# Kernel optimization log

Measured on AMD Instinct MI355X. Metric: run time of the kernel, lower is better.

## Reference

```python
import jax, jax.numpy as jnp
import numpy as np

SIZE = 512          # framebuffer resolution (init kwarg `size`)
NUM_TRIS = 512      # number of triangles
EPS = 1e-9          # degenerate-triangle area threshold (matches `w < 1e-09`)


def setup_inputs() -> dict:
    key = jax.random.key(0)
    tris = jax.random.normal(key, (NUM_TRIS, 3, 3), dtype=jnp.float32)
    return {"tris": tris}


def _area2d(a, b, c):
    # signed parallelogram area: (b.x-a.x)*(c.y-a.y) - (b.y-a.y)*(c.x-a.x)
    return (b[..., 0] - a[..., 0]) * (c[..., 1] - a[..., 1]) - \
           (b[..., 1] - a[..., 1]) * (c[..., 0] - a[..., 0])


def reference(tris):
    size = SIZE
    dtype = tris.dtype
    half = jnp.asarray(size, dtype) * 0.5

    # lookup_table: pts[i, j] = (x_i, y_j), linspace(-1, 1), 'ij' indexing
    lin = jnp.linspace(-1.0, 1.0, size, dtype=dtype)
    xx, yy = jnp.meshgrid(lin, lin, indexing="ij")
    pts = jnp.stack([xx, yy], axis=-1)              # [S, S, 2]
    ii = jnp.arange(size)[:, None]                  # row index
    jj = jnp.arange(size)[None, :]                  # col index

    # zmin = min over all vertices of the z coordinate
    zmin = tris.reshape(-1, 3).min(axis=0)[2]
    zbuf0 = jnp.full((size, size), zmin, dtype=dtype)
    res0 = jnp.zeros((size, size, 4), dtype=dtype)

    def step(carry, tri):
        zbuf, res = carry
        t2 = tri[:, :2]                              # [3, 2] screen-space verts

        # AABB -> integer pixel box: clamp to [-1,1], map to [0,size], floor (long cast)
        aabb = jnp.concatenate([t2.min(axis=0), t2.max(axis=0)])  # xmin,ymin,xmax,ymax
        idx = jnp.floor((jnp.clip(aabb, -1.0, 1.0) + 1.0) * half).astype(jnp.int32)
        xmin, ymin, xmax, ymax = idx[0], idx[1], idx[2], idx[3]
        box = (ii >= xmin) & (ii < xmax) & (jj >= ymin) & (jj < ymax)

        w = _area2d(t2[0], t2[1], t2[2])
        valid = w >= EPS                              # original: skip if w < 1e-9
        ws = jnp.where(valid, w, jnp.asarray(1.0, dtype))

        # edge functions over the whole grid (the AABB slice only restricts pixels;
        # `box` reproduces that restriction exactly)
        pAB = _area2d(t2[1], pts, t2[0])
        pCB = _area2d(t2[2], pts, t2[1])
        pCA = _area2d(t2[0], pts, t2[2])
        inside = (jnp.maximum(pAB, 0.0) * jnp.maximum(pCB, 0.0) * jnp.maximum(pCA, 0.0)) > 0

        # barycentric interpolation of the 3d vertices
        w1 = pCB / ws
        w2 = pCA / ws
        w3 = 1.0 - w1 - w2
        p3 = w1[..., None] * tri[0] + w2[..., None] * tri[1] + w3[..., None] * tri[2]  # [S,S,3]

        zmsk = p3[..., 2] >= zbuf
        rmsk = inside & zmsk & box & valid

        zbuf = jnp.where(rmsk, p3[..., 2], zbuf)
        rgba = jnp.concatenate([p3, jnp.ones_like(p3[..., :1])], axis=-1)  # [S,S,4]
        res = jnp.where(rmsk[..., None], rgba, res)
        return (zbuf, res), None

    (zbuf, res), _ = jax.lax.scan(step, (zbuf0, res0), tris)
    return res
```

## Files before the change

### kernel.cpp

```cpp
#include <hip/hip_runtime.h>

#define TSIZE 512
#define NT 512
#define EPSV 1e-9f


__device__ __forceinline__ float rcp_fast(float x) {
  float r;
  asm("v_rcp_f32 %0, %1" : "=v"(r) : "v"(x));
  return r;
}

__global__ __launch_bounds__(512) void render_fused(const float* __restrict__ tris,
                                                    float4* __restrict__ out) {
  __shared__ float4 lrec[NT * 4];
  __shared__ unsigned lbY[NT];
  __shared__ float2 smrg[NT];
  __shared__ float sred[8];

  const int tid = threadIdx.x;
  const int s = blockIdx.x;
  const int i = s >> 3;
  const unsigned jw0 = (unsigned)((s & 7) << 6);
  const float delta = 2.0f / 511.0f;

  {
    const float4* g4 = (const float4*)tris;
    float4* rw4 = lrec;
    rw4[tid] = g4[tid];
    rw4[tid + 512] = g4[tid + 512];
    int i3 = tid + 1024;
    if (i3 < 1152) rw4[i3] = g4[i3];
  }
  __syncthreads();

  const float* rawf = (const float*)lrec;
  const float* tp = rawf + tid * 9;
  float v0x = tp[0], v0y = tp[1], v0z = tp[2];
  float v1x = tp[3], v1y = tp[4], v1z = tp[5];
  float v2x = tp[6], v2y = tp[7], v2z = tp[8];
  __syncthreads();

  float w = __fsub_rn(__fmul_rn(__fsub_rn(v1x, v0x), __fsub_rn(v2y, v0y)),
                      __fmul_rn(__fsub_rn(v1y, v0y), __fsub_rn(v2x, v0x)));
  bool valid = (w >= EPSV);
  float ws = valid ? w : 1.0f;
  float r2  = __fsub_rn(v0y, v1y), r3  = __fsub_rn(v0x, v1x);
  float r6  = __fsub_rn(v1y, v2y), r7  = __fsub_rn(v1x, v2x);
  float r10 = __fsub_rn(v2y, v0y), r11 = __fsub_rn(v2x, v0x);

  int xmn = 0, xmx = 0, ymn = 0, ymx = 0;
  if (valid) {
    float bxn = fminf(v0x, fminf(v1x, v2x));
    float byn = fminf(v0y, fminf(v1y, v2y));
    float bxx = fmaxf(v0x, fmaxf(v1x, v2x));
    float byx = fmaxf(v0y, fmaxf(v1y, v2y));
    xmn = (int)floorf(__fmul_rn(__fadd_rn(fminf(fmaxf(bxn, -1.0f), 1.0f), 1.0f), 256.0f));
    ymn = (int)floorf(__fmul_rn(__fadd_rn(fminf(fmaxf(byn, -1.0f), 1.0f), 1.0f), 256.0f));
    xmx = (int)floorf(__fmul_rn(__fadd_rn(fminf(fmaxf(bxx, -1.0f), 1.0f), 1.0f), 256.0f));
    ymx = (int)floorf(__fmul_rn(__fadd_rn(fminf(fmaxf(byx, -1.0f), 1.0f), 1.0f), 256.0f));
  }

  bool pass = ((unsigned)i >= (unsigned)xmn) & ((unsigned)i < (unsigned)xmx) &
              ((unsigned)ymn < jw0 + 64u) & ((unsigned)ymx > jw0);
  if (pass) {
    const float px_s = -1.0f + (float)i * delta;
    const float pyL = -1.0f + (float)jw0 * delta;
    const float pyR = -1.0f + (float)(jw0 + 63u) * delta;
    float ylo = -1e30f, yhi = 1e30f;
    {
      float S = -r3, c = (v1y * r3 - v1x * r2) + r2 * px_s;
      if (S > 1e-20f)       { float cd = -c * rcp_fast(S); ylo = fmaxf(ylo, cd - (0.005f + 4e-6f * fabsf(cd))); }
      else if (S < -1e-20f) { float cd = -c * rcp_fast(S); yhi = fminf(yhi, cd + (0.005f + 4e-6f * fabsf(cd))); }
    }
    {
      float S = -r7, c = (v2y * r7 - v2x * r6) + r6 * px_s;
      if (S > 1e-20f)       { float cd = -c * rcp_fast(S); ylo = fmaxf(ylo, cd - (0.005f + 4e-6f * fabsf(cd))); }
      else if (S < -1e-20f) { float cd = -c * rcp_fast(S); yhi = fminf(yhi, cd + (0.005f + 4e-6f * fabsf(cd))); }
    }
    {
      float S = -r11, c = (v0y * r11 - v0x * r10) + r10 * px_s;
      if (S > 1e-20f)       { float cd = -c * rcp_fast(S); ylo = fmaxf(ylo, cd - (0.005f + 4e-6f * fabsf(cd))); }
      else if (S < -1e-20f) { float cd = -c * rcp_fast(S); yhi = fminf(yhi, cd + (0.005f + 4e-6f * fabsf(cd))); }
    }
    pass = (ylo <= pyR) & (yhi >= pyL);
  }
  const unsigned long long word = __ballot(pass ? 1 : 0);

  lrec[tid * 4 + 0] = make_float4(v1x, v1y, r2, r3);
  lrec[tid * 4 + 1] = make_float4(v2x, v2y, r6, r7);
  lrec[tid * 4 + 2] = make_float4(v0x, v0y, r10, r11);
  lrec[tid * 4 + 3] = make_float4(__fdiv_rn(1.0f, ws), v2z,
                                  __fsub_rn(v0z, v2z), __fsub_rn(v1z, v2z));
  lbY[tid] = (unsigned)ymn | ((unsigned)ymx << 16);

  float zp = fminf(v0z, fminf(v1z, v2z));
  for (int off = 32; off > 0; off >>= 1) zp = fminf(zp, __shfl_down(zp, off, 64));
  if ((tid & 63) == 0) sred[tid >> 6] = zp;
  __syncthreads();
  float zm0 = sred[0];
#pragma unroll
  for (int k = 1; k < 8; ++k) zm0 = fminf(zm0, sred[k]);

  const int lane = tid & 63;
  const int base = tid & ~63;
  const unsigned ju = jw0 + (unsigned)lane;
  const float px = __fadd_rn(-1.0f, __fmul_rn((float)i, delta));
  const float py = __fadd_rn(-1.0f, __fmul_rn((float)ju, delta));

  float zb = zm0;
  int tw = -1;
  unsigned long long m = word;
  while (m) {
    const int t = base + __builtin_ctzll(m);
    m &= m - 1;
    float4 c0 = lrec[t * 4 + 0];
    float4 c1 = lrec[t * 4 + 1];
    float4 c2 = lrec[t * 4 + 2];
    float4 c3 = lrec[t * 4 + 3];
    unsigned yb = lbY[t];
    float pAB = __fsub_rn(__fmul_rn(__fsub_rn(px, c0.x), c0.z),
                          __fmul_rn(__fsub_rn(py, c0.y), c0.w));
    float pCB = __fsub_rn(__fmul_rn(__fsub_rn(px, c1.x), c1.z),
                          __fmul_rn(__fsub_rn(py, c1.y), c1.w));
    float pCA = __fsub_rn(__fmul_rn(__fsub_rn(px, c2.x), c2.z),
                          __fmul_rn(__fsub_rn(py, c2.y), c2.w));
    bool ins = (pAB > 0.0f) & (pCB > 0.0f) & (pCA > 0.0f) &
               (ju >= (yb & 0xFFFFu)) & (ju < (yb >> 16));
    float w1 = __fmul_rn(pCB, c3.x);
    float w2 = __fmul_rn(pCA, c3.x);
    float pz = __fmaf_rn(w1, c3.z, __fmaf_rn(w2, c3.w, c3.y));
    bool mk = ins & (pz >= zb);
    zb = mk ? pz : zb;
    tw = mk ? t : tw;
  }
  smrg[tid] = make_float2(zb, __int_as_float(tw));
  __syncthreads();

  if (tid < 64) {
    float2 best = smrg[tid];
    float zf = best.x;
    int twf = __float_as_int(best.y);
#pragma unroll
    for (int w8 = 1; w8 < 8; ++w8) {
      float2 c = smrg[w8 * 64 + tid];
      int tc = __float_as_int(c.y);
      bool win = (c.x > zf) | ((c.x == zf) & (tc > twf));
      zf = win ? c.x : zf;
      twf = win ? tc : twf;
    }
    float4 res = make_float4(0.0f, 0.0f, 0.0f, 0.0f);
    if (twf >= 0) {
      float4 f1 = lrec[twf * 4 + 1];
      float4 f2 = lrec[twf * 4 + 2];
      float4 f3 = lrec[twf * 4 + 3];
      float pCB = __fsub_rn(__fmul_rn(__fsub_rn(px, f1.x), f1.z),
                            __fmul_rn(__fsub_rn(py, f1.y), f1.w));
      float pCA = __fsub_rn(__fmul_rn(__fsub_rn(px, f2.x), f2.z),
                            __fmul_rn(__fsub_rn(py, f2.y), f2.w));
      float w1 = __fmul_rn(pCB, f3.x);
      float w2 = __fmul_rn(pCA, f3.x);
      float rx = __fmaf_rn(w1, -f2.w, __fmaf_rn(w2, f1.w, f1.x));
      float ry = __fmaf_rn(w1, -f2.z, __fmaf_rn(w2, f1.z, f1.y));
      res = make_float4(rx, ry, zf, 1.0f);
    }
    out[((unsigned)i << 9) | (jw0 + (unsigned)tid)] = res;
  }
}

extern "C" void kernel_launch(void* const* d_in, const int* in_sizes, int n_in,
                              void* d_out, int out_size, void* d_ws, size_t ws_size,
                              hipStream_t stream) {
  const float* tris = (const float*)d_in[0];
  float4* out = (float4*)d_out;
  hipLaunchKernelGGL(render_fused, dim3(4096), dim3(512), 0, stream, tris, out);
}
```

Baseline: 78.49 us.

## Process 256 columns per block, splitting triangles across two waves per segment

Each block now covers half a row (256 pixels, four 64-pixel segments) instead of 64 pixels. Per-triangle setup and the triangle load into shared memory are amortized over four times as many pixels, and the grid shrinks from 4096 to 1024 blocks. Two waves share each segment and each handles half the triangles, so the final depth merge compares two candidates instead of eight. In exchange, per-wave work becomes more uneven and there are fewer blocks to hide latency.

Result: faster. 70.78 us (-9.8%).

```diff
diff --git a/kernel.cpp b/kernel.cpp
--- a/kernel.cpp
+++ b/kernel.cpp
@@ -16,12 +16,14 @@
   __shared__ float4 lrec[NT * 4];
   __shared__ unsigned lbY[NT];
   __shared__ float2 smrg[NT];
+  __shared__ unsigned long long swords[32];
   __shared__ float sred[8];
 
   const int tid = threadIdx.x;
-  const int s = blockIdx.x;
-  const int i = s >> 3;
-  const unsigned jw0 = (unsigned)((s & 7) << 6);
+  const int bb = blockIdx.x;
+  const int i = bb >> 1;
+  const int jhalf = bb & 1;
+  const unsigned jbase = (unsigned)(jhalf << 8);
   const float delta = 2.0f / 511.0f;
 
   {
@@ -29,8 +31,7 @@
     float4* rw4 = lrec;
     rw4[tid] = g4[tid];
     rw4[tid + 512] = g4[tid + 512];
-    int i3 = tid + 1024;
-    if (i3 < 1152) rw4[i3] = g4[i3];
+    if (tid < 128) rw4[tid + 1024] = g4[tid + 1024];
   }
   __syncthreads();
 
@@ -61,13 +62,10 @@
     ymx = (int)floorf(__fmul_rn(__fadd_rn(fminf(fmaxf(byx, -1.0f), 1.0f), 1.0f), 256.0f));
   }
 
-  bool pass = ((unsigned)i >= (unsigned)xmn) & ((unsigned)i < (unsigned)xmx) &
-              ((unsigned)ymn < jw0 + 64u) & ((unsigned)ymx > jw0);
-  if (pass) {
+  const bool xpass = ((unsigned)i >= (unsigned)xmn) & ((unsigned)i < (unsigned)xmx);
+  float ylo = -1e30f, yhi = 1e30f;
+  if (xpass) {
     const float px_s = -1.0f + (float)i * delta;
-    const float pyL = -1.0f + (float)jw0 * delta;
-    const float pyR = -1.0f + (float)(jw0 + 63u) * delta;
-    float ylo = -1e30f, yhi = 1e30f;
     {
       float S = -r3, c = (v1y * r3 - v1x * r2) + r2 * px_s;
       if (S > 1e-20f)       { float cd = -c * rcp_fast(S); ylo = fmaxf(ylo, cd - (0.005f + 4e-6f * fabsf(cd))); }
@@ -83,9 +81,18 @@
       if (S > 1e-20f)       { float cd = -c * rcp_fast(S); ylo = fmaxf(ylo, cd - (0.005f + 4e-6f * fabsf(cd))); }
       else if (S < -1e-20f) { float cd = -c * rcp_fast(S); yhi = fminf(yhi, cd + (0.005f + 4e-6f * fabsf(cd))); }
     }
-    pass = (ylo <= pyR) & (yhi >= pyL);
   }
-  const unsigned long long word = __ballot(pass ? 1 : 0);
+
+#pragma unroll
+  for (int k = 0; k < 4; ++k) {
+    const unsigned jw0 = jbase + ((unsigned)k << 6);
+    const float pyL = -1.0f + (float)jw0 * delta;
+    const float pyR = -1.0f + (float)(jw0 + 63u) * delta;
+    bool pk = xpass & ((unsigned)ymn < jw0 + 64u) & ((unsigned)ymx > jw0) &
+              (ylo <= pyR) & (yhi >= pyL);
+    unsigned long long wd = __ballot(pk ? 1 : 0);
+    if ((tid & 63) == 0) swords[k * 8 + (tid >> 6)] = wd;
+  }
 
   lrec[tid * 4 + 0] = make_float4(v1x, v1y, r2, r3);
   lrec[tid * 4 + 1] = make_float4(v2x, v2y, r6, r7);
@@ -100,71 +107,77 @@
   __syncthreads();
   float zm0 = sred[0];
 #pragma unroll
-  for (int k = 1; k < 8; ++k) zm0 = fminf(zm0, sred[k]);
+  for (int kk = 1; kk < 8; ++kk) zm0 = fminf(zm0, sred[kk]);
 
+  const int wv = tid >> 6;
   const int lane = tid & 63;
-  const int base = tid & ~63;
-  const unsigned ju = jw0 + (unsigned)lane;
+  const int k = wv >> 1;
+  const int h = wv & 1;
+  const unsigned ju = jbase + ((unsigned)k << 6) + (unsigned)lane;
   const float px = __fadd_rn(-1.0f, __fmul_rn((float)i, delta));
   const float py = __fadd_rn(-1.0f, __fmul_rn((float)ju, delta));
 
   float zb = zm0;
   int tw = -1;
-  unsigned long long m = word;
-  while (m) {
-    const int t = base + __builtin_ctzll(m);
-    m &= m - 1;
-    float4 c0 = lrec[t * 4 + 0];
-    float4 c1 = lrec[t * 4 + 1];
-    float4 c2 = lrec[t * 4 + 2];
-    float4 c3 = lrec[t * 4 + 3];
-    unsigned yb = lbY[t];
-    float pAB = __fsub_rn(__fmul_rn(__fsub_rn(px, c0.x), c0.z),
-                          __fmul_rn(__fsub_rn(py, c0.y), c0.w));
-    float pCB = __fsub_rn(__fmul_rn(__fsub_rn(px, c1.x), c1.z),
-                          __fmul_rn(__fsub_rn(py, c1.y), c1.w));
-    float pCA = __fsub_rn(__fmul_rn(__fsub_rn(px, c2.x), c2.z),
-                          __fmul_rn(__fsub_rn(py, c2.y), c2.w));
-    bool ins = (pAB > 0.0f) & (pCB > 0.0f) & (pCA > 0.0f) &
-               (ju >= (yb & 0xFFFFu)) & (ju < (yb >> 16));
-    float w1 = __fmul_rn(pCB, c3.x);
-    float w2 = __fmul_rn(pCA, c3.x);
-    float pz = __fmaf_rn(w1, c3.z, __fmaf_rn(w2, c3.w, c3.y));
-    bool mk = ins & (pz >= zb);
-    zb = mk ? pz : zb;
-    tw = mk ? t : tw;
+#pragma unroll 1
+  for (int q = 0; q < 4; ++q) {
+    unsigned long long m = swords[k * 8 + h * 4 + q];
+    const int tb = (h * 4 + q) << 6;
+    while (m) {
+      const int t = tb + __builtin_ctzll(m);
+      m &= m - 1;
+      float4 c0 = lrec[t * 4 + 0];
+      float4 c1 = lrec[t * 4 + 1];
+      float4 c2 = lrec[t * 4 + 2];
+      float4 c3 = lrec[t * 4 + 3];
+      unsigned yb = lbY[t];
+      float pAB = __fsub_rn(__fmul_rn(__fsub_rn(px, c0.x), c0.z),
+                            __fmul_rn(__fsub_rn(py, c0.y), c0.w));
+      float pCB = __fsub_rn(__fmul_rn(__fsub_rn(px, c1.x), c1.z),
+                            __fmul_rn(__fsub_rn(py, c1.y), c1.w));
+      float pCA = __fsub_rn(__fmul_rn(__fsub_rn(px, c2.x), c2.z),
+                            __fmul_rn(__fsub_rn(py, c2.y), c2.w));
+      bool ins = (pAB > 0.0f) & (pCB > 0.0f) & (pCA > 0.0f) &
+                 (ju >= (yb & 0xFFFFu)) & (ju < (yb >> 16));
+      float w1 = __fmul_rn(pCB, c3.x);
+      float w2 = __fmul_rn(pCA, c3.x);
+      float pz = __fmaf_rn(w1, c3.z, __fmaf_rn(w2, c3.w, c3.y));
+      bool mk = ins & (pz >= zb);
+      zb = mk ? pz : zb;
+      tw = mk ? t : tw;
+    }
   }
   smrg[tid] = make_float2(zb, __int_as_float(tw));
   __syncthreads();
 
-  if (tid < 64) {
-    float2 best = smrg[tid];
-    float zf = best.x;
-    int twf = __float_as_int(best.y);
-#pragma unroll
-    for (int w8 = 1; w8 < 8; ++w8) {
-      float2 c = smrg[w8 * 64 + tid];
-      int tc = __float_as_int(c.y);
-      bool win = (c.x > zf) | ((c.x == zf) & (tc > twf));
-      zf = win ? c.x : zf;
-      twf = win ? tc : twf;
-    }
+  if (tid < 256) {
+    const int ks = tid >> 6, l = tid & 63;
+    float2 a = smrg[ks * 128 + l];
+    float2 b = smrg[ks * 128 + 64 + l];
+    int t0 = __float_as_int(a.y), t1 = __float_as_int(b.y);
+    bool win1 = (b.x > a.x) | ((b.x == a.x) & (t1 > t0));
+    int twf = win1 ? t1 : t0;
+    float zf = win1 ? b.x : a.x;
+
+    const unsigned ju2 = jbase + (unsigned)tid;
+    const float py2 = __fadd_rn(-1.0f, __fmul_rn((float)ju2, delta));
+
     float4 res = make_float4(0.0f, 0.0f, 0.0f, 0.0f);
     if (twf >= 0) {
       float4 f1 = lrec[twf * 4 + 1];
       float4 f2 = lrec[twf * 4 + 2];
       float4 f3 = lrec[twf * 4 + 3];
       float pCB = __fsub_rn(__fmul_rn(__fsub_rn(px, f1.x), f1.z),
-                            __fmul_rn(__fsub_rn(py, f1.y), f1.w));
+                            __fmul_rn(__fsub_rn(py2, f1.y), f1.w));
       float pCA = __fsub_rn(__fmul_rn(__fsub_rn(px, f2.x), f2.z),
-                            __fmul_rn(__fsub_rn(py, f2.y), f2.w));
+                            __fmul_rn(__fsub_rn(py2, f2.y), f2.w));
       float w1 = __fmul_rn(pCB, f3.x);
       float w2 = __fmul_rn(pCA, f3.x);
       float rx = __fmaf_rn(w1, -f2.w, __fmaf_rn(w2, f1.w, f1.x));
       float ry = __fmaf_rn(w1, -f2.z, __fmaf_rn(w2, f1.z, f1.y));
       res = make_float4(rx, ry, zf, 1.0f);
     }
-    out[((unsigned)i << 9) | (jw0 + (unsigned)tid)] = res;
+    out[((unsigned)i << 9) | ju2] = res;
   }
 }
 
@@ -173,5 +186,5 @@
                               hipStream_t stream) {
   const float* tris = (const float*)d_in[0];
   float4* out = (float4*)d_out;
-  hipLaunchKernelGGL(render_fused, dim3(4096), dim3(512), 0, stream, tris, out);
+  hipLaunchKernelGGL(render_fused, dim3(1024), dim3(512), 0, stream, tris, out);
 }
```
